# Kernel tuning notes

Hardware: AMD Instinct MI355X
Metric: run time of the kernel (lower is better)

## Reference

```python
import jax, jax.numpy as jnp
import numpy as np

NX, NTEST, DX, DY = 8192, 8192, 32, 32
VAR_EPS = 0.01   # params['var_eps']
L_MEAN = 8.0     # fit kernel lengthscale after l_scale adjustment
L_VAR = 8.0


def _rbf(X, Y, l):
    # pairwise squared distances: [Nx, Nq]
    d2 = (jnp.sum(X * X, axis=1)[:, None]
          + jnp.sum(Y * Y, axis=1)[None, :]
          - 2.0 * (X @ Y.T))
    return jnp.exp(-jnp.maximum(d2, 0.0) / (2.0 * l * l))


def setup_inputs() -> dict:
    key = jax.random.key(0)
    ks = jax.random.split(key, 10)
    inp = {
        'x_mu':   jax.random.normal(ks[0], (NTEST, DX), jnp.float32),
        'y_eta':  jax.random.normal(ks[1], (NTEST, DY), jnp.float32),
        'y_mean': jax.random.normal(ks[2], (NTEST, DY), jnp.float32),
        'y_var':  jax.random.normal(ks[3], (NTEST, DY), jnp.float32) * 0.1,
        'X_mean': jax.random.normal(ks[4], (NX, DX + DY), jnp.float32),
        'X_var':  jax.random.normal(ks[5], (NX, DX + 2 * DY), jnp.float32),
        'Z_mean': jax.random.normal(ks[6], (NX, DY), jnp.float32),
        'Z_var':  jax.random.normal(ks[7], (NX, DY), jnp.float32),
        # precomputed inverse Gram matrices (stand-ins with same compute pattern)
        'kXXmean_inv': jax.random.normal(ks[8], (NX, NX), jnp.float32) * 0.001,
        'kXXvar_inv':  jax.random.normal(ks[9], (NX, NX), jnp.float32) * 0.001,
    }
    return inp


def reference(x_mu, y_eta, y_mean, y_var, X_mean, X_var, Z_mean, Z_var,
              kXXmean_inv, kXXvar_inv):
    # map_mean: x_mean = [x_mu, y_mean + y_var]
    x_mean = jnp.concatenate([x_mu, y_mean + y_var], axis=1)          # [Nq, DX+DY]
    Lambda_mean = kXXmean_inv @ Z_mean                                # [Nx, DY]
    z_mean = _rbf(X_mean, x_mean, L_MEAN).T @ Lambda_mean             # [Nq, DY]

    # map_var: x_var = [x_mu, var_eps * flip(y_eta), y_mean + y_var]
    x_var = jnp.concatenate(
        [x_mu, VAR_EPS * jnp.flip(y_eta, axis=0), y_mean + y_var], axis=1)
    Lambda_var = kXXvar_inv @ Z_var                                   # [Nx, DY]
    z_var = _rbf(X_var, x_var, L_VAR).T @ Lambda_var                  # [Nq, DY]

    # transported sample: (y_mean + z_mean) + (y_var + z_var)
    return (y_mean + z_mean) + (y_var + z_var)
```

## Files before the change

kernel.cpp:

```cpp
#include <hip/hip_runtime.h>
#include <stdint.h>

#define NXR 8192
#define NQR 8192
#define DMEAN 64
#define DVAR 96
#define DYC 32

typedef float f32x4 __attribute__((ext_vector_type(4)));
typedef __bf16 bf16x8 __attribute__((ext_vector_type(8)));
typedef unsigned short us4v __attribute__((ext_vector_type(4)));

__device__ __forceinline__ unsigned short f2bf(float f) {
    union { float f; uint32_t u; } v; v.f = f;
    uint32_t r = (v.u + 0x7FFFu + ((v.u >> 16) & 1u)) >> 16;
    return (unsigned short)r;
}
__device__ __forceinline__ float bf2f(unsigned short b) {
    union { uint32_t u; float f; } v; v.u = ((uint32_t)b) << 16;
    return v.f;
}
__device__ __forceinline__ int perm_idx(int k, int c) {
    return (k >> 5) * 1024 + (c >> 4) * 512 +
           ((((k >> 3) & 3) * 16 + (c & 15)) * 8) + (k & 7);
}

typedef const __attribute__((address_space(1))) uint32_t* as1_u32p;
typedef __attribute__((address_space(3))) uint32_t* as3_u32p;
__device__ __forceinline__ void gl_lds16(const void* g, void* l) {
    __builtin_amdgcn_global_load_lds((as1_u32p)g, (as3_u32p)l, 16, 0, 0);
}

__global__ __launch_bounds__(256) void k_prep(
    const float* __restrict__ x_mu, const float* __restrict__ y_eta,
    const float* __restrict__ y_mean, const float* __restrict__ y_var,
    const float* __restrict__ X_mean, const float* __restrict__ X_var,
    const float* __restrict__ Z_mean, const float* __restrict__ Z_var,
    unsigned short* __restrict__ Qm, unsigned short* __restrict__ Qv,
    unsigned short* __restrict__ Xm, unsigned short* __restrict__ Xv,
    unsigned short* __restrict__ Zpm, unsigned short* __restrict__ Zpv,
    float* __restrict__ qn_m, float* __restrict__ qn_v,
    float* __restrict__ Xn_m, float* __restrict__ Xn_v,
    float* __restrict__ out)
{
    int w = threadIdx.x >> 6;
    int lane = threadIdx.x & 63;
    int row = blockIdx.x * 4 + w;

    float accq_m = 0.f, accq_v = 0.f;
    if (lane < 32) {
        int c = lane;
        float xm = x_mu[row * 32 + c];
        float s  = y_mean[row * 32 + c] + y_var[row * 32 + c];
        float e  = 0.01f * y_eta[(NQR - 1 - row) * 32 + c];
        unsigned short bx = f2bf(xm), bs = f2bf(s), be = f2bf(e);
        Qm[row * DMEAN + c] = bx;  Qm[row * DMEAN + 32 + c] = bs;
        Qv[row * DVAR + c] = bx;   Qv[row * DVAR + 32 + c] = be;
        Qv[row * DVAR + 64 + c] = bs;
        out[row * 32 + c] = s;
        Zpm[perm_idx(row, c)] = f2bf(Z_mean[row * 32 + c]);
        Zpv[perm_idx(row, c)] = f2bf(Z_var[row * 32 + c]);
        float fx = bf2f(bx), fs = bf2f(bs), fe = bf2f(be);
        accq_m = fx * fx + fs * fs;
        accq_v = fx * fx + fe * fe + fs * fs;
    }
    float a = X_mean[row * DMEAN + lane];
    unsigned short ba = f2bf(a);
    Xm[row * DMEAN + lane] = ba;
    float fa = bf2f(ba);
    float accx_m = fa * fa;

    float b0 = X_var[row * DVAR + lane];
    unsigned short bb0 = f2bf(b0);
    Xv[row * DVAR + lane] = bb0;
    float fb0 = bf2f(bb0);
    float accx_v = fb0 * fb0;
    if (lane < 32) {
        float b1 = X_var[row * DVAR + 64 + lane];
        unsigned short bb1 = f2bf(b1);
        Xv[row * DVAR + 64 + lane] = bb1;
        float fb1 = bf2f(bb1);
        accx_v += fb1 * fb1;
    }
    for (int o = 32; o >= 1; o >>= 1) {
        accq_m += __shfl_xor(accq_m, o, 64);
        accq_v += __shfl_xor(accq_v, o, 64);
        accx_m += __shfl_xor(accx_m, o, 64);
        accx_v += __shfl_xor(accx_v, o, 64);
    }
    if (lane == 0) {
        qn_m[row] = accq_m; qn_v[row] = accq_v;
        Xn_m[row] = accx_m; Xn_v[row] = accx_v;
    }
}

__global__ __launch_bounds__(256, 2) void k_lambda(
    const float* __restrict__ kXXm, const float* __restrict__ kXXv,
    const unsigned short* __restrict__ Zpm, const unsigned short* __restrict__ Zpv,
    unsigned short* __restrict__ Lpm, unsigned short* __restrict__ Lpv)
{
    __shared__ __align__(16) char smem[65536];
    int b = blockIdx.x;
    int mat = b & 1;
    int rg = b >> 1;
    const float* A = mat ? kXXv : kXXm;
    const unsigned short* Zp = mat ? Zpv : Zpm;
    unsigned short* Lp = mat ? Lpv : Lpm;

    int w = threadIdx.x >> 6, lane = threadIdx.x & 63;
    int r0 = rg * 16;
    char* wlds = smem + w * 16384;

    int hl = lane >> 5;
    int cb = (lane & 31) * 16;
    const char* Ag = (const char*)A + (size_t)(r0 + hl) * 32768 + w * 8192;
    const char* Zq = (const char*)Zp + (size_t)w * 131072 + lane * 16;

    int rt = lane & 15, g = lane >> 4;
    int sw = (rt & 7) << 4;
    int rd0 = w * 16384 + rt * 512 + ((g * 32) ^ sw);
    int rd1 = rd0 ^ 16;

    f32x4 acc0 = {0.f, 0.f, 0.f, 0.f}, acc1 = {0.f, 0.f, 0.f, 0.f};
    bf16x8 zA[8], zB[8];

    auto stageA = [&](int t, int slot) {
        char* d = wlds + slot;
        const char* s = Ag + (size_t)t * 512;
#pragma unroll
        for (int i = 0; i < 8; ++i) {
            int sw_i = ((2 * i + hl) & 7) << 4;
            gl_lds16(s + (size_t)i * 65536 + (cb ^ sw_i), d + i * 1024);
        }
    };
    auto loadZ = [&](bf16x8* z, int t) {
        const char* zb = Zq + (size_t)t * 8192;
#pragma unroll
        for (int kk = 0; kk < 4; ++kk) {
            z[2 * kk]     = *(const bf16x8*)(zb + kk * 2048);
            z[2 * kk + 1] = *(const bf16x8*)(zb + kk * 2048 + 1024);
        }
    };
    auto procST = [&](int slot, const bf16x8* z) {
#pragma unroll
        for (int kk = 0; kk < 4; ++kk) {
            f32x4 a0 = *(const f32x4*)(smem + rd0 + slot + kk * 128);
            f32x4 a1 = *(const f32x4*)(smem + rd1 + slot + kk * 128);
            union { unsigned short u[8]; bf16x8 v; } af;
#pragma unroll
            for (int j = 0; j < 4; ++j) { af.u[j] = f2bf(a0[j]); af.u[4 + j] = f2bf(a1[j]); }
            acc0 = __builtin_amdgcn_mfma_f32_16x16x32_bf16(af.v, z[2 * kk], acc0, 0, 0, 0);
            acc1 = __builtin_amdgcn_mfma_f32_16x16x32_bf16(af.v, z[2 * kk + 1], acc1, 0, 0, 0);
        }
    };

    stageA(0, 0);    loadZ(zA, 0);
    stageA(1, 8192); loadZ(zB, 1);
#pragma unroll 1
    for (int tt = 0; tt < 7; ++tt) {
        int t = 2 * tt;
        asm volatile("s_waitcnt vmcnt(16)" ::: "memory");
        procST(0, zA);
        asm volatile("" ::: "memory");
        stageA(t + 2, 0);   loadZ(zA, t + 2);
        asm volatile("s_waitcnt vmcnt(16)" ::: "memory");
        procST(8192, zB);
        asm volatile("" ::: "memory");
        stageA(t + 3, 8192); loadZ(zB, t + 3);
    }
    asm volatile("s_waitcnt vmcnt(16)" ::: "memory");
    procST(0, zA);
    asm volatile("s_waitcnt vmcnt(0)" ::: "memory");
    procST(8192, zB);

    __syncthreads();
    float (*red)[64][8] = (float (*)[64][8])smem;
    *(f32x4*)&red[w][lane][0] = acc0;
    *(f32x4*)&red[w][lane][4] = acc1;
    __syncthreads();
    int tix = threadIdx.x;
    int row = tix >> 4, c16 = tix & 15;
    int ls = (row >> 2) * 16 + c16;
    int rr = row & 3;
    float v0 = red[0][ls][rr] + red[1][ls][rr] + red[2][ls][rr] + red[3][ls][rr];
    float v1 = red[0][ls][4 + rr] + red[1][ls][4 + rr] +
               red[2][ls][4 + rr] + red[3][ls][4 + rr];
    Lp[perm_idx(r0 + row, c16)]      = f2bf(v0);
    Lp[perm_idx(r0 + row, c16 + 16)] = f2bf(v1);
}

__global__ __launch_bounds__(256) void k_transport(
    const unsigned short* __restrict__ Qm, const unsigned short* __restrict__ Qv,
    const unsigned short* __restrict__ Xm, const unsigned short* __restrict__ Xv,
    const float* __restrict__ qn_m, const float* __restrict__ qn_v,
    const float* __restrict__ Xn_m, const float* __restrict__ Xn_v,
    const unsigned short* __restrict__ Lpm, const unsigned short* __restrict__ Lpv,
    float* __restrict__ out)
{
    __shared__ unsigned short KT[4][16 * 40];
    int b = blockIdx.x;
    int mat = b & 1;
    int split = (b >> 1) & 3;
    int qb = b >> 3;
    const unsigned short* Q = mat ? Qv : Qm;
    const unsigned short* X = mat ? Xv : Xm;
    const float* qn = mat ? qn_v : qn_m;
    const float* Xn = mat ? Xn_v : Xn_m;
    const unsigned short* Lp = mat ? Lpv : Lpm;
    const int D = mat ? DVAR : DMEAN;
    const int nk0 = mat ? 3 : 2;

    int w = threadIdx.x >> 6, lane = threadIdx.x & 63;
    int q0 = qb * 64 + w * 16;
    int qrow = q0 + (lane & 15);
    int g = lane >> 4;

    bf16x8 Qf[3];
    for (int c0 = 0; c0 < nk0; ++c0)
        Qf[c0] = *(const bf16x8*)(Q + (size_t)qrow * D + c0 * 32 + g * 8);
    float qn_c = qn[qrow];
    unsigned short* lds = KT[w];

    f32x4 z0 = {0.f, 0.f, 0.f, 0.f}, z1 = {0.f, 0.f, 0.f, 0.f};
    for (int xb = 0; xb < 64; ++xb) {
        int x0 = split * 2048 + xb * 32;
#pragma unroll
        for (int sub = 0; sub < 2; ++sub) {
            int xrow = x0 + sub * 16 + (lane & 15);
            const unsigned short* Xr = X + (size_t)xrow * D + g * 8;
            f32x4 s = {0.f, 0.f, 0.f, 0.f};
            s = __builtin_amdgcn_mfma_f32_16x16x32_bf16(*(const bf16x8*)(Xr), Qf[0], s, 0, 0, 0);
            s = __builtin_amdgcn_mfma_f32_16x16x32_bf16(*(const bf16x8*)(Xr + 32), Qf[1], s, 0, 0, 0);
            if (nk0 == 3)
                s = __builtin_amdgcn_mfma_f32_16x16x32_bf16(*(const bf16x8*)(Xr + 64), Qf[2], s, 0, 0, 0);
            int xnb = x0 + sub * 16 + g * 4;
            f32x4 xn4 = *(const f32x4*)(Xn + xnb);
            us4v kv;
#pragma unroll
            for (int r = 0; r < 4; ++r) {
                float d2 = xn4[r] + qn_c - 2.0f * s[r];
                d2 = fmaxf(d2, 0.0f);
                kv[r] = f2bf(__expf(-d2 * 0.0078125f));
            }
            *(us4v*)(lds + (lane & 15) * 40 + sub * 16 + g * 4) = kv;
        }
        asm volatile("s_waitcnt lgkmcnt(0)" ::: "memory");
        bf16x8 Kf = *(const bf16x8*)(lds + (lane & 15) * 40 + g * 8);
        const unsigned short* lpb = Lp + (size_t)(x0 >> 5) * 1024 + lane * 8;
        bf16x8 l0 = *(const bf16x8*)(lpb);
        bf16x8 l1 = *(const bf16x8*)(lpb + 512);
        z0 = __builtin_amdgcn_mfma_f32_16x16x32_bf16(Kf, l0, z0, 0, 0, 0);
        z1 = __builtin_amdgcn_mfma_f32_16x16x32_bf16(Kf, l1, z1, 0, 0, 0);
    }
    int rbase = q0 + g * 4;
    int c0 = lane & 15;
#pragma unroll
    for (int r = 0; r < 4; ++r) {
        atomicAdd(&out[(rbase + r) * 32 + c0], z0[r]);
        atomicAdd(&out[(rbase + r) * 32 + c0 + 16], z1[r]);
    }
}

extern "C" void kernel_launch(void* const* d_in, const int* in_sizes, int n_in,
                              void* d_out, int out_size, void* d_ws, size_t ws_size,
                              hipStream_t stream) {
    const float* x_mu   = (const float*)d_in[0];
    const float* y_eta  = (const float*)d_in[1];
    const float* y_mean = (const float*)d_in[2];
    const float* y_var  = (const float*)d_in[3];
    const float* X_mean = (const float*)d_in[4];
    const float* X_var  = (const float*)d_in[5];
    const float* Z_mean = (const float*)d_in[6];
    const float* Z_var  = (const float*)d_in[7];
    const float* kXXm   = (const float*)d_in[8];
    const float* kXXv   = (const float*)d_in[9];
    float* out = (float*)d_out;

    char* ws = (char*)d_ws;
    size_t off = 0;
    auto carve = [&](size_t bytes) { char* p = ws + off; off += (bytes + 255) & ~(size_t)255; return p; };
    unsigned short* Qm  = (unsigned short*)carve(NQR * DMEAN * 2);
    unsigned short* Qv  = (unsigned short*)carve(NQR * DVAR * 2);
    unsigned short* Xm  = (unsigned short*)carve(NXR * DMEAN * 2);
    unsigned short* Xv  = (unsigned short*)carve(NXR * DVAR * 2);
    unsigned short* Zpm = (unsigned short*)carve(NXR * DYC * 2);
    unsigned short* Zpv = (unsigned short*)carve(NXR * DYC * 2);
    unsigned short* Lpm = (unsigned short*)carve(NXR * DYC * 2);
    unsigned short* Lpv = (unsigned short*)carve(NXR * DYC * 2);
    float* qn_m = (float*)carve(NQR * 4);
    float* qn_v = (float*)carve(NQR * 4);
    float* Xn_m = (float*)carve(NXR * 4);
    float* Xn_v = (float*)carve(NXR * 4);

    k_prep<<<dim3(2048), dim3(256), 0, stream>>>(
        x_mu, y_eta, y_mean, y_var, X_mean, X_var, Z_mean, Z_var,
        Qm, Qv, Xm, Xv, Zpm, Zpv, qn_m, qn_v, Xn_m, Xn_v, out);
    k_lambda<<<dim3(1024), dim3(256), 0, stream>>>(kXXm, kXXv, Zpm, Zpv, Lpm, Lpv);
    k_transport<<<dim3(1024), dim3(256), 0, stream>>>(
        Qm, Qv, Xm, Xv, qn_m, qn_v, Xn_m, Xn_v, Lpm, Lpv, out);
}
```

Measured before the change: 687.4 us.

## Software-pipeline X, Lambda and norm loads with double-buffered registers in transport kernel

Restructures the transport loop so that the X rows, permuted Lambda fragments and X norms for the next 32-row tile are loaded into registers while the current tile's MFMAs and exp run. It alternates two register sets and two LDS staging buffers. Launch bounds now request 3 blocks per SM. This hides global-load latency behind compute at the cost of more VGPRs. The last iteration wraps around and issues one redundant prefetch.

After: 679.9 us. About the same (-1.1%).

```diff
diff --git a/kernel.cpp b/kernel.cpp
--- a/kernel.cpp
+++ b/kernel.cpp
@@ -189,7 +189,7 @@
     Lp[perm_idx(r0 + row, c16 + 16)] = f2bf(v1);
 }
 
-__global__ __launch_bounds__(256) void k_transport(
+__global__ __launch_bounds__(256, 3) void k_transport(
     const unsigned short* __restrict__ Qm, const unsigned short* __restrict__ Qv,
     const unsigned short* __restrict__ Xm, const unsigned short* __restrict__ Xv,
     const float* __restrict__ qn_m, const float* __restrict__ qn_v,
@@ -197,7 +197,7 @@
     const unsigned short* __restrict__ Lpm, const unsigned short* __restrict__ Lpv,
     float* __restrict__ out)
 {
-    __shared__ unsigned short KT[4][16 * 40];
+    __shared__ unsigned short KT[4][2][16 * 40];
     int b = blockIdx.x;
     int mat = b & 1;
     int split = (b >> 1) & 3;
@@ -219,26 +219,45 @@
     for (int c0 = 0; c0 < nk0; ++c0)
         Qf[c0] = *(const bf16x8*)(Q + (size_t)qrow * D + c0 * 32 + g * 8);
     float qn_c = qn[qrow];
-    unsigned short* lds = KT[w];
 
     f32x4 z0 = {0.f, 0.f, 0.f, 0.f}, z1 = {0.f, 0.f, 0.f, 0.f};
-    for (int xb = 0; xb < 64; ++xb) {
-        int x0 = split * 2048 + xb * 32;
+
+    bf16x8 xA[6], xB[6];
+    bf16x8 lpA[2], lpB[2];
+    f32x4  xnA[2], xnB[2];
+
+    auto loadX = [&](bf16x8* xf, int t) {
+        int x0 = split * 2048 + (t & 63) * 32;
 #pragma unroll
         for (int sub = 0; sub < 2; ++sub) {
             int xrow = x0 + sub * 16 + (lane & 15);
             const unsigned short* Xr = X + (size_t)xrow * D + g * 8;
+            xf[sub * 3 + 0] = *(const bf16x8*)(Xr);
+            xf[sub * 3 + 1] = *(const bf16x8*)(Xr + 32);
+            if (nk0 == 3) xf[sub * 3 + 2] = *(const bf16x8*)(Xr + 64);
+        }
+    };
+    auto loadAux = [&](bf16x8* lp, f32x4* xn, int t) {
+        int x0 = split * 2048 + (t & 63) * 32;
+        const unsigned short* lpb = Lp + (size_t)(x0 >> 5) * 1024 + lane * 8;
+        lp[0] = *(const bf16x8*)(lpb);
+        lp[1] = *(const bf16x8*)(lpb + 512);
+        xn[0] = *(const f32x4*)(Xn + x0 + g * 4);
+        xn[1] = *(const f32x4*)(Xn + x0 + 16 + g * 4);
+    };
+    auto phase = [&](const bf16x8* xf, const bf16x8* lp, const f32x4* xn,
+                     unsigned short* lds) {
+#pragma unroll
+        for (int sub = 0; sub < 2; ++sub) {
             f32x4 s = {0.f, 0.f, 0.f, 0.f};
-            s = __builtin_amdgcn_mfma_f32_16x16x32_bf16(*(const bf16x8*)(Xr), Qf[0], s, 0, 0, 0);
-            s = __builtin_amdgcn_mfma_f32_16x16x32_bf16(*(const bf16x8*)(Xr + 32), Qf[1], s, 0, 0, 0);
+            s = __builtin_amdgcn_mfma_f32_16x16x32_bf16(xf[sub * 3 + 0], Qf[0], s, 0, 0, 0);
+            s = __builtin_amdgcn_mfma_f32_16x16x32_bf16(xf[sub * 3 + 1], Qf[1], s, 0, 0, 0);
             if (nk0 == 3)
-                s = __builtin_amdgcn_mfma_f32_16x16x32_bf16(*(const bf16x8*)(Xr + 64), Qf[2], s, 0, 0, 0);
-            int xnb = x0 + sub * 16 + g * 4;
-            f32x4 xn4 = *(const f32x4*)(Xn + xnb);
+                s = __builtin_amdgcn_mfma_f32_16x16x32_bf16(xf[sub * 3 + 2], Qf[2], s, 0, 0, 0);
             us4v kv;
 #pragma unroll
             for (int r = 0; r < 4; ++r) {
-                float d2 = xn4[r] + qn_c - 2.0f * s[r];
+                float d2 = xn[sub][r] + qn_c - 2.0f * s[r];
                 d2 = fmaxf(d2, 0.0f);
                 kv[r] = f2bf(__expf(-d2 * 0.0078125f));
             }
@@ -246,12 +265,20 @@
         }
         asm volatile("s_waitcnt lgkmcnt(0)" ::: "memory");
         bf16x8 Kf = *(const bf16x8*)(lds + (lane & 15) * 40 + g * 8);
-        const unsigned short* lpb = Lp + (size_t)(x0 >> 5) * 1024 + lane * 8;
-        bf16x8 l0 = *(const bf16x8*)(lpb);
-        bf16x8 l1 = *(const bf16x8*)(lpb + 512);
-        z0 = __builtin_amdgcn_mfma_f32_16x16x32_bf16(Kf, l0, z0, 0, 0, 0);
-        z1 = __builtin_amdgcn_mfma_f32_16x16x32_bf16(Kf, l1, z1, 0, 0, 0);
-    }
+        z0 = __builtin_amdgcn_mfma_f32_16x16x32_bf16(Kf, lp[0], z0, 0, 0, 0);
+        z1 = __builtin_amdgcn_mfma_f32_16x16x32_bf16(Kf, lp[1], z1, 0, 0, 0);
+    };
+
+    loadX(xA, 0); loadAux(lpA, xnA, 0);
+#pragma unroll 1
+    for (int i = 0; i < 32; ++i) {
+        int t = 2 * i;
+        loadX(xB, t + 1); loadAux(lpB, xnB, t + 1);
+        phase(xA, lpA, xnA, KT[w][0]);
+        loadX(xA, t + 2); loadAux(lpA, xnA, t + 2);
+        phase(xB, lpB, xnB, KT[w][1]);
+    }
+
     int rbase = q0 + g * 4;
     int c0 = lane & 15;
 #pragma unroll
```
